# Optimization experiments

Measured on AMD Instinct MI355X. Metric: run time of the kernel, lower is better.

Reference implementation:

```python
import jax, jax.numpy as jnp
import numpy as np

C = 128          # in_channels == dim (ratio 1)
S = 16           # patch_size == stride (non-overlapping)
TEMP = float(np.sqrt(C))  # temp = dim ** 0.5


def setup_inputs() -> dict:
    key = jax.random.key(0)
    ks = jax.random.split(key, 9)
    x = jax.random.normal(ks[0], (2, C, 512, 512), dtype=jnp.float32)
    std = 0.01
    # 1x1 conv weights (out, in) and biases; conv_out is normal-init here to
    # make the reference non-trivial (zeros_init would zero the branch).
    Wq = jax.random.normal(ks[1], (C, C), dtype=jnp.float32) * std
    bq = jax.random.normal(ks[2], (C,), dtype=jnp.float32) * std
    Wk = jax.random.normal(ks[3], (C, C), dtype=jnp.float32) * std
    bk = jax.random.normal(ks[4], (C,), dtype=jnp.float32) * std
    Wv = jax.random.normal(ks[5], (C, C), dtype=jnp.float32) * std
    bv = jax.random.normal(ks[6], (C,), dtype=jnp.float32) * std
    Wo = jax.random.normal(ks[7], (C, C), dtype=jnp.float32) * std
    bo = jax.random.normal(ks[8], (C,), dtype=jnp.float32) * std
    return {"x": x, "Wq": Wq, "bq": bq, "Wk": Wk, "bk": bk,
            "Wv": Wv, "bv": bv, "Wo": Wo, "bo": bo}


def reference(x, Wq, bq, Wk, bk, Wv, bv, Wo, bo):
    B, Cc, H, W = x.shape
    gh, gw = H // S, W // S
    N = gh * gw
    L = S * S  # tokens per patch
    # Unfold into non-overlapping patches; H,W divisible by S so pad=0,
    # attention mask is all-zero and fold overlap scalar is all-one.
    # Patch column order of nn.Unfold is row-major over (gh, gw);
    # token order inside a patch is row-major (sh, sw).
    p = (x.reshape(B, Cc, gh, S, gw, S)
           .transpose(0, 2, 4, 1, 3, 5)
           .reshape(B * N, Cc, L))            # (n, C, L)
    q = jnp.einsum('dc,ncl->nld', Wq, p) + bq  # (n, L, d)
    k = jnp.einsum('dc,ncl->ndl', Wk, p) + bk[:, None]  # (n, d, L)
    attn = jax.nn.softmax(jnp.einsum('nld,ndm->nlm', q, k) / TEMP, axis=-1)
    v = jnp.einsum('dc,ncl->nld', Wv, p) + bv  # (n, L, d)
    y = jnp.einsum('nlm,nmd->nld', attn, v)    # (n, L, d)
    y = jnp.einsum('cd,nld->ncl', Wo, y) + bo[:, None]  # conv_out
    out = p + y  # identity residual
    # Fold back (non-overlapping -> pure reshape; scalar == 1 everywhere)
    out = (out.reshape(B, gh, gw, Cc, S, S)
              .transpose(0, 3, 1, 4, 2, 5)
              .reshape(B, Cc, H, W))
    return out
```

## Files before the change

### kernel.cpp

```cpp
#include <hip/hip_runtime.h>

typedef __attribute__((ext_vector_type(8))) short bf16x8;
typedef __attribute__((ext_vector_type(4))) float f32x4;

#define LDS_STRIDE 136
#define INV_TEMP 0.08838834764831845f

static __device__ __forceinline__ unsigned short f2b(float f) {
    union { float f; unsigned int u; } v; v.f = f;
    unsigned int b = (v.u + 0x7fffu + ((v.u >> 16) & 1u)) >> 16;
    return (unsigned short)b;
}
static __device__ __forceinline__ float b2f(unsigned short s) {
    union { float f; unsigned int u; } v; v.u = ((unsigned int)s) << 16;
    return v.f;
}

__global__ void prep_weights(const float* __restrict__ Wq, const float* __restrict__ Wk,
                             const float* __restrict__ Wv, const float* __restrict__ Wo,
                             unsigned short* __restrict__ wbf) {
    int i = blockIdx.x * 256 + threadIdx.x;
    wbf[i]          = f2b(Wq[i]);
    wbf[16384 + i]  = f2b(Wk[i]);
    wbf[32768 + i]  = f2b(Wv[i]);
    wbf[49152 + i]  = f2b(Wo[i]);
}

__launch_bounds__(512, 2)
__global__ void patch_attn(const float* __restrict__ x,
                           const float* __restrict__ bq, const float* __restrict__ bk,
                           const float* __restrict__ bv, const float* __restrict__ bo,
                           const unsigned short* __restrict__ wbf,
                           float* __restrict__ out)
{
    __shared__ __align__(16) unsigned short sPT[256 * LDS_STRIDE];
    __shared__ __align__(16) unsigned char  sUN[72704];

    const int tid  = threadIdx.x;
    const int w    = tid >> 6;
    const int lane = tid & 63;
    const int quad = lane >> 4;
    const int l16  = lane & 15;
    const int dcol = w * 16 + l16;

    const int pid = blockIdx.x;
    const int b   = pid >> 10;
    const int n   = pid & 1023;
    const int gy  = n >> 5, gx = n & 31;
    const long patch_off = ((long)(b * 128) * 512 + gy * 16) * 512 + gx * 16;

    const unsigned short* Wq_bf = wbf;
    const unsigned short* Wk_bf = wbf + 16384;
    const unsigned short* Wv_bf = wbf + 32768;
    const unsigned short* Wo_bf = wbf + 49152;

    {
        const int dc = lane & 3, g = lane >> 2;
        const int l0 = ((w & 3) * 16 + g) * 4;
        const int sh = l0 >> 4, sw = l0 & 15;
        const int cbh = tid >> 8;
        for (int it = 0; it < 16; ++it) {
            const int c0 = (it * 2 + cbh) * 4;
            const float4 f = *(const float4*)(x + patch_off + ((long)(c0 + dc) * 512 + sh) * 512 + sw);
            unsigned int A = (unsigned int)f2b(f.x) | ((unsigned int)f2b(f.y) << 16);
            unsigned int B = (unsigned int)f2b(f.z) | ((unsigned int)f2b(f.w) << 16);
            unsigned int Pa = __shfl_xor(A, 1);
            unsigned int Pb = __shfl_xor(B, 1);
            unsigned int A1 = (dc & 1) ? ((Pa >> 16) | (A & 0xffff0000u))
                                       : ((A & 0x0000ffffu) | (Pa << 16));
            unsigned int B1 = (dc & 1) ? ((Pb >> 16) | (B & 0xffff0000u))
                                       : ((B & 0x0000ffffu) | (Pb << 16));
            unsigned int Ra = __shfl_xor(A1, 2);
            unsigned int Rb = __shfl_xor(B1, 2);
            uint2 o;
            o.x = (dc & 2) ? Rb : A1;
            o.y = (dc & 2) ? B1 : Ra;
            *(uint2*)&sPT[(l0 + dc) * LDS_STRIDE + c0] = o;
        }
    }
    __syncthreads();

    unsigned short* qscr = (unsigned short*)sUN;
    {
        bf16x8 wq[4];
#pragma unroll
        for (int ks = 0; ks < 4; ++ks)
            wq[ks] = *(const bf16x8*)(Wq_bf + dcol * 128 + ks * 32 + quad * 8);
        const float qb = bq[dcol];
#pragma unroll
        for (int lt = 0; lt < 16; ++lt) {
            f32x4 acc = {0.f, 0.f, 0.f, 0.f};
#pragma unroll
            for (int ks = 0; ks < 4; ++ks) {
                bf16x8 a = *(const bf16x8*)&sPT[(lt * 16 + l16) * LDS_STRIDE + ks * 32 + quad * 8];
                acc = __builtin_amdgcn_mfma_f32_16x16x32_bf16(a, wq[ks], acc, 0, 0, 0);
            }
#pragma unroll
            for (int r = 0; r < 4; ++r)
                qscr[(lt * 16 + quad * 4 + r) * LDS_STRIDE + dcol] = f2b((acc[r] + qb) * INV_TEMP);
        }
    }
    __syncthreads();
    const int lbase = w * 32;
    bf16x8 qfrag[2][4];
#pragma unroll
    for (int lt = 0; lt < 2; ++lt)
#pragma unroll
        for (int ks = 0; ks < 4; ++ks)
            qfrag[lt][ks] = *(const bf16x8*)&qscr[(lbase + lt * 16 + l16) * LDS_STRIDE + ks * 32 + quad * 8];
    __syncthreads();

    unsigned short* kTc = (unsigned short*)sUN;
    unsigned short* vTc = (unsigned short*)(sUN + 17408);
    unsigned short* Pw  = (unsigned short*)(sUN + 35840) + w * (32 * 72);

    bf16x8 wk[4], wv[4];
#pragma unroll
    for (int ks = 0; ks < 4; ++ks) {
        wk[ks] = *(const bf16x8*)(Wk_bf + dcol * 128 + ks * 32 + quad * 8);
        wv[ks] = *(const bf16x8*)(Wv_bf + dcol * 128 + ks * 32 + quad * 8);
    }
    const float kb = bk[dcol], vb = bv[dcol];

    f32x4 O[2][8];
#pragma unroll
    for (int lt = 0; lt < 2; ++lt)
#pragma unroll
        for (int dt = 0; dt < 8; ++dt) O[lt][dt] = (f32x4){0.f, 0.f, 0.f, 0.f};
    float mrow[2][4], lrow[2][4];
#pragma unroll
    for (int lt = 0; lt < 2; ++lt)
#pragma unroll
        for (int r = 0; r < 4; ++r) { mrow[lt][r] = -1e30f; lrow[lt][r] = 0.f; }

    for (int ch = 0; ch < 4; ++ch) {
        const int m0 = ch * 64;
#pragma unroll
        for (int mt = 0; mt < 4; ++mt) {
            bf16x8 a[4];
#pragma unroll
            for (int ks = 0; ks < 4; ++ks)
                a[ks] = *(const bf16x8*)&sPT[(m0 + mt * 16 + l16) * LDS_STRIDE + ks * 32 + quad * 8];
            f32x4 kacc = {0.f, 0.f, 0.f, 0.f}, vacc = {0.f, 0.f, 0.f, 0.f};
#pragma unroll
            for (int ks = 0; ks < 4; ++ks) {
                kacc = __builtin_amdgcn_mfma_f32_16x16x32_bf16(a[ks], wk[ks], kacc, 0, 0, 0);
                vacc = __builtin_amdgcn_mfma_f32_16x16x32_bf16(a[ks], wv[ks], vacc, 0, 0, 0);
            }
#pragma unroll
            for (int r = 0; r < 4; ++r)
                kTc[(mt * 16 + quad * 4 + r) * LDS_STRIDE + dcol] = f2b(kacc[r] + kb);
            unsigned short vp[4];
#pragma unroll
            for (int r = 0; r < 4; ++r) vp[r] = f2b(vacc[r] + vb);
            unsigned long long pk = (unsigned long long)vp[0]
                                  | ((unsigned long long)vp[1] << 16)
                                  | ((unsigned long long)vp[2] << 32)
                                  | ((unsigned long long)vp[3] << 48);
            *(unsigned long long*)&vTc[dcol * 72 + mt * 16 + quad * 4] = pk;
        }
        __syncthreads();

#pragma unroll
        for (int lt = 0; lt < 2; ++lt) {
            f32x4 s[4];
#pragma unroll
            for (int nt = 0; nt < 4; ++nt) {
                f32x4 acc = {0.f, 0.f, 0.f, 0.f};
#pragma unroll
                for (int ks = 0; ks < 4; ++ks) {
                    bf16x8 bb = *(const bf16x8*)&kTc[(nt * 16 + l16) * LDS_STRIDE + ks * 32 + quad * 8];
                    acc = __builtin_amdgcn_mfma_f32_16x16x32_bf16(qfrag[lt][ks], bb, acc, 0, 0, 0);
                }
                s[nt] = acc;
            }
            float mx[4];
#pragma unroll
            for (int r = 0; r < 4; ++r) {
                float m = fmaxf(fmaxf(s[0][r], s[1][r]), fmaxf(s[2][r], s[3][r]));
#pragma unroll
                for (int off = 8; off; off >>= 1) m = fmaxf(m, __shfl_xor(m, off));
                mx[r] = m;
            }
            bool need = false;
#pragma unroll
            for (int r = 0; r < 4; ++r) need |= (mx[r] - mrow[lt][r] > 8.f);
            if (__any(need)) {
#pragma unroll
                for (int r = 0; r < 4; ++r) {
                    float mnew  = fmaxf(mrow[lt][r], mx[r]);
                    float alpha = __expf(mrow[lt][r] - mnew);
                    mrow[lt][r] = mnew;
                    lrow[lt][r] *= alpha;
#pragma unroll
                    for (int dt = 0; dt < 8; ++dt) O[lt][dt][r] *= alpha;
                }
            }
#pragma unroll
            for (int r = 0; r < 4; ++r) {
                float rs = 0.f;
#pragma unroll
                for (int nt = 0; nt < 4; ++nt) {
                    float p = __expf(s[nt][r] - mrow[lt][r]);
                    s[nt][r] = p;
                    rs += p;
                }
#pragma unroll
                for (int off = 8; off; off >>= 1) rs += __shfl_xor(rs, off);
                lrow[lt][r] += rs;
            }
#pragma unroll
            for (int nt = 0; nt < 4; ++nt)
#pragma unroll
                for (int r = 0; r < 4; ++r)
                    Pw[(lt * 16 + quad * 4 + r) * 72 + nt * 16 + l16] = f2b(s[nt][r]);
#pragma unroll
            for (int dt = 0; dt < 8; ++dt) {
                f32x4 acc = O[lt][dt];
#pragma unroll
                for (int kt = 0; kt < 2; ++kt) {
                    bf16x8 pa = *(const bf16x8*)&Pw[(lt * 16 + l16) * 72 + kt * 32 + quad * 8];
                    bf16x8 vv = *(const bf16x8*)&vTc[(dt * 16 + l16) * 72 + kt * 32 + quad * 8];
                    acc = __builtin_amdgcn_mfma_f32_16x16x32_bf16(pa, vv, acc, 0, 0, 0);
                }
                O[lt][dt] = acc;
            }
        }
        __syncthreads();
    }

    unsigned short* yA = (unsigned short*)sUN;
#pragma unroll
    for (int lt = 0; lt < 2; ++lt) {
        float inv[4];
#pragma unroll
        for (int r = 0; r < 4; ++r) inv[r] = 1.f / lrow[lt][r];
#pragma unroll
        for (int dt = 0; dt < 8; ++dt)
#pragma unroll
            for (int r = 0; r < 4; ++r)
                yA[(lbase + lt * 16 + quad * 4 + r) * LDS_STRIDE + dt * 16 + l16] =
                    f2b(O[lt][dt][r] * inv[r]);
    }
    __syncthreads();

    {
        bf16x8 wo[4];
#pragma unroll
        for (int ks = 0; ks < 4; ++ks)
            wo[ks] = *(const bf16x8*)(Wo_bf + dcol * 128 + ks * 32 + quad * 8);
        const float ob = bo[dcol];
        float* outc = out + patch_off + (long)dcol * 262144;
#pragma unroll
        for (int lt = 0; lt < 16; ++lt) {
            f32x4 acc = {0.f, 0.f, 0.f, 0.f};
#pragma unroll
            for (int ks = 0; ks < 4; ++ks) {
                bf16x8 a = *(const bf16x8*)&yA[(lt * 16 + l16) * LDS_STRIDE + ks * 32 + quad * 8];
                acc = __builtin_amdgcn_mfma_f32_16x16x32_bf16(a, wo[ks], acc, 0, 0, 0);
            }
            f32x4 o4;
#pragma unroll
            for (int r = 0; r < 4; ++r)
                o4[r] = acc[r] + ob + b2f(sPT[(lt * 16 + quad * 4 + r) * LDS_STRIDE + dcol]);
            *(f32x4*)(outc + lt * 512 + quad * 4) = o4;
        }
    }
}

extern "C" void kernel_launch(void* const* d_in, const int* in_sizes, int n_in,
                              void* d_out, int out_size, void* d_ws, size_t ws_size,
                              hipStream_t stream) {
    (void)in_sizes; (void)n_in; (void)out_size; (void)ws_size;
    const float* x  = (const float*)d_in[0];
    const float* Wq = (const float*)d_in[1];
    const float* bq = (const float*)d_in[2];
    const float* Wk = (const float*)d_in[3];
    const float* bk = (const float*)d_in[4];
    const float* Wv = (const float*)d_in[5];
    const float* bv = (const float*)d_in[6];
    const float* Wo = (const float*)d_in[7];
    const float* bo = (const float*)d_in[8];
    unsigned short* wbf = (unsigned short*)d_ws;

    prep_weights<<<64, 256, 0, stream>>>(Wq, Wk, Wv, Wo, wbf);
    patch_attn<<<2048, 512, 0, stream>>>(x, bq, bk, bv, bo, wbf, (float*)d_out);
}
```

Before: 698.1 us.

## Double waves per block to 16, each owning 16 query rows

The patch attention kernel now launches 1024-thread blocks. Each of the 16 waves owns a 16-row slice of queries instead of 32, and pairs of waves split each 16-channel column block for the Q, K/V and output projections. This halves the per-wave accumulator and softmax state, which lowers register pressure and lets twice as many waves be resident per CU on the same LDS footprint, so latency is better hidden. The cost is that the per-chunk block-wide barriers now synchronize 16 waves instead of 8, and the register budget under the tighter launch bound is smaller.

```diff
diff --git a/kernel.cpp b/kernel.cpp
--- a/kernel.cpp
+++ b/kernel.cpp
@@ -26,7 +26,7 @@
     wbf[49152 + i]  = f2b(Wo[i]);
 }
 
-__launch_bounds__(512, 2)
+__launch_bounds__(1024, 4)
 __global__ void patch_attn(const float* __restrict__ x,
                            const float* __restrict__ bq, const float* __restrict__ bk,
                            const float* __restrict__ bv, const float* __restrict__ bo,
@@ -41,7 +41,9 @@
     const int lane = tid & 63;
     const int quad = lane >> 4;
     const int l16  = lane & 15;
-    const int dcol = w * 16 + l16;
+    const int half = w & 1;
+    const int dcol = (w >> 1) * 16 + l16;
+    const int lbase = w * 16;
 
     const int pid = blockIdx.x;
     const int b   = pid >> 10;
@@ -58,9 +60,9 @@
         const int dc = lane & 3, g = lane >> 2;
         const int l0 = ((w & 3) * 16 + g) * 4;
         const int sh = l0 >> 4, sw = l0 & 15;
-        const int cbh = tid >> 8;
-        for (int it = 0; it < 16; ++it) {
-            const int c0 = (it * 2 + cbh) * 4;
+        const int cbh = w >> 2;
+        for (int it = 0; it < 8; ++it) {
+            const int c0 = (it * 4 + cbh) * 4;
             const float4 f = *(const float4*)(x + patch_off + ((long)(c0 + dc) * 512 + sh) * 512 + sw);
             unsigned int A = (unsigned int)f2b(f.x) | ((unsigned int)f2b(f.y) << 16);
             unsigned int B = (unsigned int)f2b(f.z) | ((unsigned int)f2b(f.w) << 16);
@@ -88,7 +90,8 @@
             wq[ks] = *(const bf16x8*)(Wq_bf + dcol * 128 + ks * 32 + quad * 8);
         const float qb = bq[dcol];
 #pragma unroll
-        for (int lt = 0; lt < 16; ++lt) {
+        for (int lt8 = 0; lt8 < 8; ++lt8) {
+            const int lt = half * 8 + lt8;
             f32x4 acc = {0.f, 0.f, 0.f, 0.f};
 #pragma unroll
             for (int ks = 0; ks < 4; ++ks) {
@@ -101,18 +104,15 @@
         }
     }
     __syncthreads();
-    const int lbase = w * 32;
-    bf16x8 qfrag[2][4];
-#pragma unroll
-    for (int lt = 0; lt < 2; ++lt)
-#pragma unroll
-        for (int ks = 0; ks < 4; ++ks)
-            qfrag[lt][ks] = *(const bf16x8*)&qscr[(lbase + lt * 16 + l16) * LDS_STRIDE + ks * 32 + quad * 8];
+    bf16x8 qfrag[4];
+#pragma unroll
+    for (int ks = 0; ks < 4; ++ks)
+        qfrag[ks] = *(const bf16x8*)&qscr[(lbase + l16) * LDS_STRIDE + ks * 32 + quad * 8];
     __syncthreads();
 
     unsigned short* kTc = (unsigned short*)sUN;
     unsigned short* vTc = (unsigned short*)(sUN + 17408);
-    unsigned short* Pw  = (unsigned short*)(sUN + 35840) + w * (32 * 72);
+    unsigned short* Pw  = (unsigned short*)(sUN + 35840) + w * (16 * 72);
 
     bf16x8 wk[4], wv[4];
 #pragma unroll
@@ -122,21 +122,18 @@
     }
     const float kb = bk[dcol], vb = bv[dcol];
 
-    f32x4 O[2][8];
-#pragma unroll
-    for (int lt = 0; lt < 2; ++lt)
-#pragma unroll
-        for (int dt = 0; dt < 8; ++dt) O[lt][dt] = (f32x4){0.f, 0.f, 0.f, 0.f};
-    float mrow[2][4], lrow[2][4];
-#pragma unroll
-    for (int lt = 0; lt < 2; ++lt)
-#pragma unroll
-        for (int r = 0; r < 4; ++r) { mrow[lt][r] = -1e30f; lrow[lt][r] = 0.f; }
+    f32x4 O[8];
+#pragma unroll
+    for (int dt = 0; dt < 8; ++dt) O[dt] = (f32x4){0.f, 0.f, 0.f, 0.f};
+    float mrow[4], lrow[4];
+#pragma unroll
+    for (int r = 0; r < 4; ++r) { mrow[r] = -1e30f; lrow[r] = 0.f; }
 
     for (int ch = 0; ch < 4; ++ch) {
         const int m0 = ch * 64;
 #pragma unroll
-        for (int mt = 0; mt < 4; ++mt) {
+        for (int mt2 = 0; mt2 < 2; ++mt2) {
+            const int mt = half * 2 + mt2;
             bf16x8 a[4];
 #pragma unroll
             for (int ks = 0; ks < 4; ++ks)
@@ -161,8 +158,7 @@
         }
         __syncthreads();
 
-#pragma unroll
-        for (int lt = 0; lt < 2; ++lt) {
+        {
             f32x4 s[4];
 #pragma unroll
             for (int nt = 0; nt < 4; ++nt) {
@@ -170,7 +166,7 @@
 #pragma unroll
                 for (int ks = 0; ks < 4; ++ks) {
                     bf16x8 bb = *(const bf16x8*)&kTc[(nt * 16 + l16) * LDS_STRIDE + ks * 32 + quad * 8];
-                    acc = __builtin_amdgcn_mfma_f32_16x16x32_bf16(qfrag[lt][ks], bb, acc, 0, 0, 0);
+                    acc = __builtin_amdgcn_mfma_f32_16x16x32_bf16(qfrag[ks], bb, acc, 0, 0, 0);
                 }
                 s[nt] = acc;
             }
@@ -184,16 +180,16 @@
             }
             bool need = false;
 #pragma unroll
-            for (int r = 0; r < 4; ++r) need |= (mx[r] - mrow[lt][r] > 8.f);
+            for (int r = 0; r < 4; ++r) need |= (mx[r] - mrow[r] > 8.f);
             if (__any(need)) {
 #pragma unroll
                 for (int r = 0; r < 4; ++r) {
-                    float mnew  = fmaxf(mrow[lt][r], mx[r]);
-                    float alpha = __expf(mrow[lt][r] - mnew);
-                    mrow[lt][r] = mnew;
-                    lrow[lt][r] *= alpha;
-#pragma unroll
-                    for (int dt = 0; dt < 8; ++dt) O[lt][dt][r] *= alpha;
+                    float mnew  = fmaxf(mrow[r], mx[r]);
+                    float alpha = __expf(mrow[r] - mnew);
+                    mrow[r] = mnew;
+                    lrow[r] *= alpha;
+#pragma unroll
+                    for (int dt = 0; dt < 8; ++dt) O[dt][r] *= alpha;
                 }
             }
 #pragma unroll
@@ -201,46 +197,45 @@
                 float rs = 0.f;
 #pragma unroll
                 for (int nt = 0; nt < 4; ++nt) {
-                    float p = __expf(s[nt][r] - mrow[lt][r]);
+                    float p = __expf(s[nt][r] - mrow[r]);
                     s[nt][r] = p;
                     rs += p;
                 }
 #pragma unroll
                 for (int off = 8; off; off >>= 1) rs += __shfl_xor(rs, off);
-                lrow[lt][r] += rs;
+                lrow[r] += rs;
             }
 #pragma unroll
             for (int nt = 0; nt < 4; ++nt)
 #pragma unroll
                 for (int r = 0; r < 4; ++r)
-                    Pw[(lt * 16 + quad * 4 + r) * 72 + nt * 16 + l16] = f2b(s[nt][r]);
+                    Pw[(quad * 4 + r) * 72 + nt * 16 + l16] = f2b(s[nt][r]);
 #pragma unroll
             for (int dt = 0; dt < 8; ++dt) {
-                f32x4 acc = O[lt][dt];
+                f32x4 acc = O[dt];
 #pragma unroll
                 for (int kt = 0; kt < 2; ++kt) {
-                    bf16x8 pa = *(const bf16x8*)&Pw[(lt * 16 + l16) * 72 + kt * 32 + quad * 8];
+                    bf16x8 pa = *(const bf16x8*)&Pw[l16 * 72 + kt * 32 + quad * 8];
                     bf16x8 vv = *(const bf16x8*)&vTc[(dt * 16 + l16) * 72 + kt * 32 + quad * 8];
                     acc = __builtin_amdgcn_mfma_f32_16x16x32_bf16(pa, vv, acc, 0, 0, 0);
                 }
-                O[lt][dt] = acc;
+                O[dt] = acc;
             }
         }
         __syncthreads();
     }
 
     unsigned short* yA = (unsigned short*)sUN;
-#pragma unroll
-    for (int lt = 0; lt < 2; ++lt) {
+    {
         float inv[4];
 #pragma unroll
-        for (int r = 0; r < 4; ++r) inv[r] = 1.f / lrow[lt][r];
+        for (int r = 0; r < 4; ++r) inv[r] = 1.f / lrow[r];
 #pragma unroll
         for (int dt = 0; dt < 8; ++dt)
 #pragma unroll
             for (int r = 0; r < 4; ++r)
-                yA[(lbase + lt * 16 + quad * 4 + r) * LDS_STRIDE + dt * 16 + l16] =
-                    f2b(O[lt][dt][r] * inv[r]);
+                yA[(lbase + quad * 4 + r) * LDS_STRIDE + dt * 16 + l16] =
+                    f2b(O[dt][r] * inv[r]);
     }
     __syncthreads();
 
@@ -252,7 +247,8 @@
         const float ob = bo[dcol];
         float* outc = out + patch_off + (long)dcol * 262144;
 #pragma unroll
-        for (int lt = 0; lt < 16; ++lt) {
+        for (int lt8 = 0; lt8 < 8; ++lt8) {
+            const int lt = half * 8 + lt8;
             f32x4 acc = {0.f, 0.f, 0.f, 0.f};
 #pragma unroll
             for (int ks = 0; ks < 4; ++ks) {
@@ -284,5 +280,5 @@
     unsigned short* wbf = (unsigned short*)d_ws;
 
     prep_weights<<<64, 256, 0, stream>>>(Wq, Wk, Wv, Wo, wbf);
-    patch_attn<<<2048, 512, 0, stream>>>(x, bq, bk, bv, bo, wbf, (float*)d_out);
-}
+    patch_attn<<<2048, 1024, 0, stream>>>(x, bq, bk, bv, bo, wbf, (float*)d_out);
+}
```

New measurement: 772.8 us. +10.7%, slower.

## Software-pipeline K/V projection for the next chunk ahead of the attention compute

Applied to the files above, without the earlier changes.

The K/V projection MFMAs for the next 64-token chunk now run before the current chunk's QK^T/softmax/PV step. Their bf16-packed results are held in registers and written to LDS at the top of the next iteration, so the projection overlaps the attention math and the first chunk overlaps the Q projection tail. This raises register pressure (packed K/V plus fully unrolled chunk loop) under launch_bounds(512,2), which could cause spills or lower occupancy.

```diff
diff --git a/kernel.cpp b/kernel.cpp
--- a/kernel.cpp
+++ b/kernel.cpp
@@ -42,6 +42,7 @@
     const int quad = lane >> 4;
     const int l16  = lane & 15;
     const int dcol = w * 16 + l16;
+    const int lbase = w * 32;
 
     const int pid = blockIdx.x;
     const int b   = pid >> 10;
@@ -80,6 +81,37 @@
     }
     __syncthreads();
 
+    bf16x8 wk[4], wv[4];
+#pragma unroll
+    for (int ks = 0; ks < 4; ++ks) {
+        wk[ks] = *(const bf16x8*)(Wk_bf + dcol * 128 + ks * 32 + quad * 8);
+        wv[ks] = *(const bf16x8*)(Wv_bf + dcol * 128 + ks * 32 + quad * 8);
+    }
+    const float kb = bk[dcol], vb = bv[dcol];
+
+    unsigned int kp01[4], kp23[4];
+    unsigned long long vpk[4];
+
+#define BUILD_KV(M0)                                                              \
+    {                                                                             \
+        _Pragma("unroll")                                                         \
+        for (int mt = 0; mt < 4; ++mt) {                                          \
+            f32x4 kacc = {0.f, 0.f, 0.f, 0.f}, vacc = {0.f, 0.f, 0.f, 0.f};       \
+            _Pragma("unroll")                                                     \
+            for (int ks = 0; ks < 4; ++ks) {                                      \
+                bf16x8 a = *(const bf16x8*)&sPT[((M0) + mt * 16 + l16) * LDS_STRIDE + ks * 32 + quad * 8]; \
+                kacc = __builtin_amdgcn_mfma_f32_16x16x32_bf16(a, wk[ks], kacc, 0, 0, 0); \
+                vacc = __builtin_amdgcn_mfma_f32_16x16x32_bf16(a, wv[ks], vacc, 0, 0, 0); \
+            }                                                                     \
+            kp01[mt] = (unsigned int)f2b(kacc[0] + kb) | ((unsigned int)f2b(kacc[1] + kb) << 16); \
+            kp23[mt] = (unsigned int)f2b(kacc[2] + kb) | ((unsigned int)f2b(kacc[3] + kb) << 16); \
+            vpk[mt]  = (unsigned long long)f2b(vacc[0] + vb)                      \
+                     | ((unsigned long long)f2b(vacc[1] + vb) << 16)              \
+                     | ((unsigned long long)f2b(vacc[2] + vb) << 32)              \
+                     | ((unsigned long long)f2b(vacc[3] + vb) << 48);             \
+        }                                                                         \
+    }
+
     unsigned short* qscr = (unsigned short*)sUN;
     {
         bf16x8 wq[4];
@@ -100,8 +132,8 @@
                 qscr[(lt * 16 + quad * 4 + r) * LDS_STRIDE + dcol] = f2b((acc[r] + qb) * INV_TEMP);
         }
     }
+    BUILD_KV(0);
     __syncthreads();
-    const int lbase = w * 32;
     bf16x8 qfrag[2][4];
 #pragma unroll
     for (int lt = 0; lt < 2; ++lt)
@@ -114,14 +146,6 @@
     unsigned short* vTc = (unsigned short*)(sUN + 17408);
     unsigned short* Pw  = (unsigned short*)(sUN + 35840) + w * (32 * 72);
 
-    bf16x8 wk[4], wv[4];
-#pragma unroll
-    for (int ks = 0; ks < 4; ++ks) {
-        wk[ks] = *(const bf16x8*)(Wk_bf + dcol * 128 + ks * 32 + quad * 8);
-        wv[ks] = *(const bf16x8*)(Wv_bf + dcol * 128 + ks * 32 + quad * 8);
-    }
-    const float kb = bk[dcol], vb = bv[dcol];
-
     f32x4 O[2][8];
 #pragma unroll
     for (int lt = 0; lt < 2; ++lt)
@@ -133,33 +157,20 @@
 #pragma unroll
         for (int r = 0; r < 4; ++r) { mrow[lt][r] = -1e30f; lrow[lt][r] = 0.f; }
 
+#pragma unroll
     for (int ch = 0; ch < 4; ++ch) {
-        const int m0 = ch * 64;
 #pragma unroll
         for (int mt = 0; mt < 4; ++mt) {
-            bf16x8 a[4];
-#pragma unroll
-            for (int ks = 0; ks < 4; ++ks)
-                a[ks] = *(const bf16x8*)&sPT[(m0 + mt * 16 + l16) * LDS_STRIDE + ks * 32 + quad * 8];
-            f32x4 kacc = {0.f, 0.f, 0.f, 0.f}, vacc = {0.f, 0.f, 0.f, 0.f};
-#pragma unroll
-            for (int ks = 0; ks < 4; ++ks) {
-                kacc = __builtin_amdgcn_mfma_f32_16x16x32_bf16(a[ks], wk[ks], kacc, 0, 0, 0);
-                vacc = __builtin_amdgcn_mfma_f32_16x16x32_bf16(a[ks], wv[ks], vacc, 0, 0, 0);
-            }
-#pragma unroll
-            for (int r = 0; r < 4; ++r)
-                kTc[(mt * 16 + quad * 4 + r) * LDS_STRIDE + dcol] = f2b(kacc[r] + kb);
-            unsigned short vp[4];
-#pragma unroll
-            for (int r = 0; r < 4; ++r) vp[r] = f2b(vacc[r] + vb);
-            unsigned long long pk = (unsigned long long)vp[0]
-                                  | ((unsigned long long)vp[1] << 16)
-                                  | ((unsigned long long)vp[2] << 32)
-                                  | ((unsigned long long)vp[3] << 48);
-            *(unsigned long long*)&vTc[dcol * 72 + mt * 16 + quad * 4] = pk;
+            const int row = mt * 16 + quad * 4;
+            kTc[(row + 0) * LDS_STRIDE + dcol] = (unsigned short)(kp01[mt]);
+            kTc[(row + 1) * LDS_STRIDE + dcol] = (unsigned short)(kp01[mt] >> 16);
+            kTc[(row + 2) * LDS_STRIDE + dcol] = (unsigned short)(kp23[mt]);
+            kTc[(row + 3) * LDS_STRIDE + dcol] = (unsigned short)(kp23[mt] >> 16);
+            *(unsigned long long*)&vTc[dcol * 72 + mt * 16 + quad * 4] = vpk[mt];
         }
         __syncthreads();
+
+        if (ch < 3) BUILD_KV((ch + 1) * 64);
 
 #pragma unroll
         for (int lt = 0; lt < 2; ++lt) {
@@ -228,6 +239,7 @@
         }
         __syncthreads();
     }
+#undef BUILD_KV
 
     unsigned short* yA = (unsigned short*)sUN;
 #pragma unroll
```

Result: no change. 694.6 us (-0.5%).
